# Kernel optimization log

Measured on AMD Instinct MI355X. Metric: run time of the kernel, lower is better.

Reference implementation:

```python
import jax, jax.numpy as jnp
import numpy as np

SCALING = 2.0  # lora_alpha / r


def setup_inputs() -> dict:
    key = jax.random.key(0)
    ks = jax.random.split(key, 6)
    B, S, D_IN, D_OUT, R = 4, 4096, 4096, 4096, 32
    x = jax.random.normal(ks[0], (B, S, D_IN), dtype=jnp.float32)
    W = jax.random.normal(ks[1], (D_OUT, D_IN), dtype=jnp.float32) * 0.02
    b = jax.random.normal(ks[2], (D_OUT,), dtype=jnp.float32) * 0.02
    A = jax.random.normal(ks[3], (R, D_IN), dtype=jnp.float32) * 0.02
    B_w = jax.random.normal(ks[4], (D_OUT, R), dtype=jnp.float32) * 0.02
    # per-sample activation offsets, in [1, S]
    alora_offsets = jax.random.randint(ks[5], (B,), 1, S + 1, dtype=jnp.int32)
    return {"x": x, "alora_offsets": alora_offsets, "W": W, "b": b, "A": A, "B_w": B_w}


def reference(x, alora_offsets, W, b, A, B_w):
    # base linear: y = x @ W^T + b
    base = jnp.einsum("bsd,od->bso", x, W) + b  # [B, S, D_OUT]
    # LoRA path on full sequence (dropout is identity at inference, p=0)
    lora = jnp.einsum("bsr,or->bso", jnp.einsum("bsd,rd->bsr", x, A), B_w) * SCALING
    # per-sample tail mask: only last k = min(offset, S) positions get the LoRA update
    S = x.shape[1]
    k = jnp.minimum(alora_offsets, S)  # [B]
    pos = jnp.arange(S, dtype=jnp.int32)
    mask = pos[None, :] >= (S - k)[:, None]  # [B, S] True on the tail
    return base + jnp.where(mask[:, :, None], lora, jnp.zeros((), base.dtype))
```

## Files before the change

### kernel.cpp

```cpp
#include <hip/hip_runtime.h>
#include <hip/hip_bf16.h>

typedef __attribute__((ext_vector_type(8))) short short8;
typedef __attribute__((ext_vector_type(4))) float f32x4;

#define GLOAD_LDS16(gp, lp)                                                      \
  __builtin_amdgcn_global_load_lds(                                              \
      (const __attribute__((address_space(1))) void*)(gp),                       \
      (__attribute__((address_space(3))) void*)(lp), 16, 0, 0)

#define SBAR() asm volatile("s_barrier" ::: "memory")
#define VMC(n)                                                                   \
  do {                                                                           \
    asm volatile("s_waitcnt vmcnt(" #n ")" ::: "memory");                        \
    __builtin_amdgcn_sched_barrier(0);                                           \
  } while (0)

__device__ __forceinline__ unsigned short f2bf_rne(float f) {
  union { float f; unsigned int u; } v; v.f = f;
  unsigned int u = v.u;
  u += 0x7fffu + ((u >> 16) & 1u);
  return (unsigned short)(u >> 16);
}

__device__ __forceinline__ short8 pack8(f32x4 a, f32x4 b) {
  short8 o;
  o[0] = (short)f2bf_rne(a[0]); o[1] = (short)f2bf_rne(a[1]);
  o[2] = (short)f2bf_rne(a[2]); o[3] = (short)f2bf_rne(a[3]);
  o[4] = (short)f2bf_rne(b[0]); o[5] = (short)f2bf_rne(b[1]);
  o[6] = (short)f2bf_rne(b[2]); o[7] = (short)f2bf_rne(b[3]);
  return o;
}

__global__ void cvt_f32_bf16(const float* __restrict__ src,
                             unsigned short* __restrict__ dst, int n8) {
  int i = blockIdx.x * blockDim.x + threadIdx.x;
  int stride = gridDim.x * blockDim.x;
  const f32x4* s4 = (const f32x4*)src;
  short8* d8 = (short8*)dst;
  for (; i < n8; i += stride) {
    d8[i] = pack8(s4[2 * i], s4[2 * i + 1]);
  }
}

__global__ __launch_bounds__(256) void cvt_lora_kernel(
    const float* __restrict__ x,
    const float* __restrict__ A,
    const float* __restrict__ W,
    const int* __restrict__ offs,
    unsigned short* __restrict__ xb,
    unsigned short* __restrict__ Wb,
    unsigned short* __restrict__ T)
{
  __shared__ unsigned short xs[32 * 72];
  __shared__ unsigned short as_[32 * 72];
  const int t = threadIdx.x;
  const int m0 = blockIdx.x * 32;
  const int l = t & 63, w = t >> 6;
  const int wr = w >> 1, wc = w & 1;
  const int lr = l & 15, lk = (l >> 4) * 8;
  const int arow = t >> 3, acol = (t & 7) * 8;
  f32x4 acc = {0, 0, 0, 0};
  for (int kt = 0; kt < 64; ++kt) {
    const int kof = kt * 64 + acol;
    const float* px = x + (size_t)(m0 + arow) * 4096 + kof;
    const float* pa = A + (size_t)arow * 4096 + kof;
    short8 s0 = pack8(*(const f32x4*)px, *(const f32x4*)(px + 4));
    short8 sa = pack8(*(const f32x4*)pa, *(const f32x4*)(pa + 4));
    *(short8*)(xb + (size_t)(m0 + arow) * 4096 + kof) = s0;
    __syncthreads();
    *(short8*)&xs[arow * 72 + acol]  = s0;
    *(short8*)&as_[arow * 72 + acol] = sa;
    __syncthreads();
#pragma unroll
    for (int kk = 0; kk < 2; ++kk) {
      short8 a = *(const short8*)&xs[(wr * 16 + lr) * 72 + kk * 32 + lk];
      short8 b = *(const short8*)&as_[(wc * 16 + lr) * 72 + kk * 32 + lk];
      acc = __builtin_amdgcn_mfma_f32_16x16x32_bf16(a, b, acc, 0, 0, 0);
    }
  }
  const int rowb = (l >> 4) * 4;
#pragma unroll
  for (int j = 0; j < 4; ++j) {
    int m = m0 + wr * 16 + rowb + j;
    int bb = m >> 12, s = m & 4095;
    int kcut = offs[bb]; if (kcut > 4096) kcut = 4096;
    bool keep = s >= 4096 - kcut;
    T[(size_t)m * 32 + wc * 16 + lr] = keep ? f2bf_rne(2.0f * acc[j]) : (unsigned short)0;
  }
  const f32x4* s4 = (const f32x4*)W;
  short8* d8 = (short8*)Wb;
  const int base = blockIdx.x * 4096;
#pragma unroll
  for (int q = 0; q < 16; ++q) {
    int idx = base + q * 256 + t;
    d8[idx] = pack8(s4[2 * idx], s4[2 * idx + 1]);
  }
}

__global__ __launch_bounds__(512, 2) void gemm_kernel(
    const unsigned short* __restrict__ xb,
    const unsigned short* __restrict__ Wb,
    const unsigned short* __restrict__ Tm,
    const unsigned short* __restrict__ Bwb,
    const float* __restrict__ bias,
    float* __restrict__ out)
{
  constexpr int K = 4096;
  extern __shared__ char smem[];

  const int bid = blockIdx.x;
  const int swz = (bid & 7) * 128 + (bid >> 3);
  const int m0 = (swz >> 4) * 256;
  const int n0 = (swz & 15) * 256;

  const int t = threadIdx.x;
  const int l = t & 63, w = t >> 6;
  const int wqr = w >> 2;
  const int pr = (w >> 1) & 1;
  const int pc = w & 1;
  const int lr = l & 15, hi = l >> 4;
  const int e0 = (hi ^ (lr & 7)) * 8;

  const int srow = t >> 3;
  const int schunk = ((t & 7) ^ ((t >> 3) & 7)) * 8;
  const unsigned short* pA0 = xb + (size_t)(m0 + srow) * K + schunk;
  const unsigned short* pA1 = xb + (size_t)(m0 + 128 + srow) * K + schunk;
  const unsigned short* pB0 = Wb + (size_t)(n0 + srow) * K + schunk;
  const unsigned short* pB1 = Wb + (size_t)(n0 + 128 + srow) * K + schunk;
  unsigned short* sm = (unsigned short*)smem;
  const int ldst = t * 16;

#define STG(PTR, SLOT, ISB, HALF, KT)                                           \
  do {                                                                          \
    const unsigned short* g_ = (PTR) + (KT) * 64;                               \
    char* d_ = smem + (SLOT) * 65536 + (ISB) * 32768 + (HALF) * 16384 + ldst;   \
    GLOAD_LDS16(g_, d_);                                                        \
    GLOAD_LDS16(g_ + (size_t)64 * K, d_ + 8192);                                \
  } while (0)

  f32x4 acc[2][4][4];
  short8 afr[4];

  {
    const unsigned short* tp = Tm + (size_t)(m0 + wqr * 128 + pr * 64 + lr) * 32 + hi * 8;
    short8 la[4];
#pragma unroll
    for (int i = 0; i < 4; ++i) la[i] = *(const short8*)(tp + i * 512);
    short8 lb[2][4];
#pragma unroll
    for (int qc = 0; qc < 2; ++qc)
#pragma unroll
      for (int j = 0; j < 4; ++j)
        lb[qc][j] = *(const short8*)(Bwb + (size_t)(n0 + qc * 128 + pc * 64 + j * 16 + lr) * 32 + hi * 8);
#pragma unroll
    for (int qc = 0; qc < 2; ++qc)
#pragma unroll
      for (int i = 0; i < 4; ++i)
#pragma unroll
        for (int j = 0; j < 4; ++j)
          acc[qc][i][j] = __builtin_amdgcn_mfma_f32_16x16x32_bf16(
              la[i], lb[qc][j], (f32x4){0.f, 0.f, 0.f, 0.f}, 0, 0, 0);
  }

  STG(pB1, 0, 1, 1, 0);
  STG(pA0, 0, 0, 0, 0);
  STG(pA1, 0, 0, 1, 0);
  STG(pB0, 0, 1, 0, 0);
  STG(pB0, 1, 1, 0, 1);
  VMC(2);
  SBAR();

#define PHASE(SLOT, QC, KK, READA, STG_STMT, WAIT_STMT)                         \
  {                                                                             \
    const unsigned short* Ah = sm + (SLOT) * 32768 + wqr * 8192;                \
    const unsigned short* Bh = sm + (SLOT) * 32768 + 16384 + (QC) * 8192;       \
    const int ek = e0 ^ ((KK) * 32);                                            \
    if (READA) {                                                                \
      _Pragma("unroll")                                                         \
      for (int i = 0; i < 4; ++i)                                               \
        afr[i] = *(const short8*)(Ah + (pr * 64 + i * 16 + lr) * 64 + ek);      \
    }                                                                           \
    short8 bfr[4];                                                              \
    _Pragma("unroll")                                                           \
    for (int j = 0; j < 4; ++j)                                                 \
      bfr[j] = *(const short8*)(Bh + (pc * 64 + j * 16 + lr) * 64 + ek);        \
    STG_STMT;                                                                   \
    SBAR();                                                                     \
    __builtin_amdgcn_s_setprio(1);                                              \
    _Pragma("unroll")                                                           \
    for (int i = 0; i < 4; ++i)                                                 \
      _Pragma("unroll")                                                         \
      for (int j = 0; j < 4; ++j)                                               \
        acc[QC][i][j] = __builtin_amdgcn_mfma_f32_16x16x32_bf16(                \
            afr[i], bfr[j], acc[QC][i][j], 0, 0, 0);                            \
    __builtin_amdgcn_s_setprio(0);                                              \
    WAIT_STMT;                                                                  \
    SBAR();                                                                     \
  }

  for (int I = 0; I < 31; ++I) {
    const int a = 2 * I;
    PHASE(0, 0, 0, 1, STG(pB1, 1, 1, 1, a + 1), ((void)0));
    PHASE(0, 1, 0, 0, STG(pA0, 1, 0, 0, a + 1), ((void)0));
    PHASE(0, 0, 1, 1, STG(pA1, 1, 0, 1, a + 1), ((void)0));
    PHASE(0, 1, 1, 0, STG(pB0, 0, 1, 0, a + 2), VMC(2));
    PHASE(1, 0, 0, 1, STG(pB1, 0, 1, 1, a + 2), ((void)0));
    PHASE(1, 1, 0, 0, STG(pA0, 0, 0, 0, a + 2), ((void)0));
    PHASE(1, 0, 1, 1, STG(pA1, 0, 0, 1, a + 2), ((void)0));
    PHASE(1, 1, 1, 0, STG(pB0, 1, 1, 0, a + 3), VMC(2));
  }
  PHASE(0, 0, 0, 1, STG(pB1, 1, 1, 1, 63), ((void)0));
  PHASE(0, 1, 0, 0, STG(pA0, 1, 0, 0, 63), ((void)0));
  PHASE(0, 0, 1, 1, STG(pA1, 1, 0, 1, 63), ((void)0));
  PHASE(0, 1, 1, 0, ((void)0), VMC(0));
  PHASE(1, 0, 0, 1, ((void)0), ((void)0));
  PHASE(1, 1, 0, 0, ((void)0), ((void)0));
  PHASE(1, 0, 1, 1, ((void)0), ((void)0));
  PHASE(1, 1, 1, 0, ((void)0), ((void)0));
#undef PHASE
#undef STG

  float bv[2][4];
#pragma unroll
  for (int qc = 0; qc < 2; ++qc)
#pragma unroll
    for (int j = 0; j < 4; ++j)
      bv[qc][j] = bias[n0 + qc * 128 + pc * 64 + j * 16 + lr];
  const int rowb = hi * 4;
#pragma unroll
  for (int qc = 0; qc < 2; ++qc)
#pragma unroll
    for (int i = 0; i < 4; ++i)
#pragma unroll
      for (int e = 0; e < 4; ++e) {
        int row = m0 + wqr * 128 + pr * 64 + i * 16 + rowb + e;
        float* orow = out + (size_t)row * 4096 + n0 + qc * 128 + pc * 64;
#pragma unroll
        for (int j = 0; j < 4; ++j) orow[j * 16 + lr] = acc[qc][i][j][e] + bv[qc][j];
      }
}

extern "C" void kernel_launch(void* const* d_in, const int* in_sizes, int n_in,
                              void* d_out, int out_size, void* d_ws, size_t ws_size,
                              hipStream_t stream) {
  const float* x   = (const float*)d_in[0];
  const int* offs  = (const int*)d_in[1];
  const float* W   = (const float*)d_in[2];
  const float* b   = (const float*)d_in[3];
  const float* A   = (const float*)d_in[4];
  const float* Bw  = (const float*)d_in[5];
  float* out = (float*)d_out;

  char* ws = (char*)d_ws;
  unsigned short* xb  = (unsigned short*)ws;
  unsigned short* Wb  = (unsigned short*)(ws + 134217728);
  unsigned short* Bwb = (unsigned short*)(ws + 167772160);
  unsigned short* T   = (unsigned short*)(ws + 168034304);

  hipFuncSetAttribute((const void*)gemm_kernel,
                      hipFuncAttributeMaxDynamicSharedMemorySize, 131072);

  cvt_f32_bf16<<<64, 256, 0, stream>>>(Bw, Bwb, 131072 / 8);
  cvt_lora_kernel<<<512, 256, 0, stream>>>(x, A, W, offs, xb, Wb, T);
  gemm_kernel<<<1024, 512, 131072, stream>>>(xb, Wb, T, Bwb, b, out);
}
```

Before: 581.4 us.

## Fuse B_w conversion into cvt_lora, prefetch x/A loads, drop setprio

```diff
diff --git a/kernel.cpp b/kernel.cpp
--- a/kernel.cpp
+++ b/kernel.cpp
@@ -32,24 +32,15 @@
   return o;
 }
 
-__global__ void cvt_f32_bf16(const float* __restrict__ src,
-                             unsigned short* __restrict__ dst, int n8) {
-  int i = blockIdx.x * blockDim.x + threadIdx.x;
-  int stride = gridDim.x * blockDim.x;
-  const f32x4* s4 = (const f32x4*)src;
-  short8* d8 = (short8*)dst;
-  for (; i < n8; i += stride) {
-    d8[i] = pack8(s4[2 * i], s4[2 * i + 1]);
-  }
-}
-
 __global__ __launch_bounds__(256) void cvt_lora_kernel(
     const float* __restrict__ x,
     const float* __restrict__ A,
     const float* __restrict__ W,
+    const float* __restrict__ Bw,
     const int* __restrict__ offs,
     unsigned short* __restrict__ xb,
     unsigned short* __restrict__ Wb,
+    unsigned short* __restrict__ Bwb,
     unsigned short* __restrict__ T)
 {
   __shared__ unsigned short xs[32 * 72];
@@ -60,14 +51,28 @@
   const int wr = w >> 1, wc = w & 1;
   const int lr = l & 15, lk = (l >> 4) * 8;
   const int arow = t >> 3, acol = (t & 7) * 8;
+
+  if (blockIdx.x < 64) {
+    int idx = blockIdx.x * 256 + t;
+    const f32x4* s4b = (const f32x4*)Bw;
+    ((short8*)Bwb)[idx] = pack8(s4b[2 * idx], s4b[2 * idx + 1]);
+  }
+
+  const float* px = x + (size_t)(m0 + arow) * 4096 + acol;
+  const float* pa = A + (size_t)arow * 4096 + acol;
+  f32x4 vx0 = *(const f32x4*)px, vx1 = *(const f32x4*)(px + 4);
+  f32x4 va0 = *(const f32x4*)pa, va1 = *(const f32x4*)(pa + 4);
+
   f32x4 acc = {0, 0, 0, 0};
   for (int kt = 0; kt < 64; ++kt) {
-    const int kof = kt * 64 + acol;
-    const float* px = x + (size_t)(m0 + arow) * 4096 + kof;
-    const float* pa = A + (size_t)arow * 4096 + kof;
-    short8 s0 = pack8(*(const f32x4*)px, *(const f32x4*)(px + 4));
-    short8 sa = pack8(*(const f32x4*)pa, *(const f32x4*)(pa + 4));
-    *(short8*)(xb + (size_t)(m0 + arow) * 4096 + kof) = s0;
+    short8 s0 = pack8(vx0, vx1);
+    short8 sa = pack8(va0, va1);
+    if (kt < 63) {
+      px += 64; pa += 64;
+      vx0 = *(const f32x4*)px; vx1 = *(const f32x4*)(px + 4);
+      va0 = *(const f32x4*)pa; va1 = *(const f32x4*)(pa + 4);
+    }
+    *(short8*)(xb + (size_t)(m0 + arow) * 4096 + kt * 64 + acol) = s0;
     __syncthreads();
     *(short8*)&xs[arow * 72 + acol]  = s0;
     *(short8*)&as_[arow * 72 + acol] = sa;
@@ -187,14 +192,12 @@
       bfr[j] = *(const short8*)(Bh + (pc * 64 + j * 16 + lr) * 64 + ek);        \
     STG_STMT;                                                                   \
     SBAR();                                                                     \
-    __builtin_amdgcn_s_setprio(1);                                              \
     _Pragma("unroll")                                                           \
     for (int i = 0; i < 4; ++i)                                                 \
       _Pragma("unroll")                                                         \
       for (int j = 0; j < 4; ++j)                                               \
         acc[QC][i][j] = __builtin_amdgcn_mfma_f32_16x16x32_bf16(                \
             afr[i], bfr[j], acc[QC][i][j], 0, 0, 0);                            \
-    __builtin_amdgcn_s_setprio(0);                                              \
     WAIT_STMT;                                                                  \
     SBAR();                                                                     \
   }
@@ -261,7 +264,6 @@
   hipFuncSetAttribute((const void*)gemm_kernel,
                       hipFuncAttributeMaxDynamicSharedMemorySize, 131072);
 
-  cvt_f32_bf16<<<64, 256, 0, stream>>>(Bw, Bwb, 131072 / 8);
-  cvt_lora_kernel<<<512, 256, 0, stream>>>(x, A, W, offs, xb, Wb, T);
+  cvt_lora_kernel<<<512, 256, 0, stream>>>(x, A, W, Bw, offs, xb, Wb, Bwb, T);
   gemm_kernel<<<1024, 512, 131072, stream>>>(xb, Wb, T, Bwb, b, out);
 }
```

Measured after the change: 583.8 us. No clear change (+0.4%).
